# Performance work log

Measured on AMD Instinct MI355X. Metric: run time of the kernel, lower is better.

Reference implementation:

```python
import jax, jax.numpy as jnp
import numpy as np

EMB = 768
HEADS = 12
HEAD_DIM = EMB // HEADS


def setup_inputs() -> dict:
    key = jax.random.key(0)
    k1, k2, k3, k4 = jax.random.split(key, 4)
    x = jax.random.normal(k1, (8, 1024, EMB), dtype=jnp.float32)
    # Dense kernels, TF default glorot-ish scale approximated with small normals
    w_qkv = jax.random.normal(k2, (EMB, 3 * EMB), dtype=jnp.float32) * 0.02
    w_out = jax.random.normal(k3, (EMB, EMB), dtype=jnp.float32) * 0.02
    b_out = jnp.zeros((EMB,), dtype=jnp.float32)
    return {"x": x, "w_qkv": w_qkv, "w_out": w_out, "b_out": b_out}


def reference(x, w_qkv, w_out, b_out):
    B, S, E = x.shape
    qkv = jnp.einsum("bse,ef->bsf", x, w_qkv)                 # [B,S,3E]
    qkv = qkv.reshape(B, S, 3, HEADS, HEAD_DIM)
    qkv = jnp.transpose(qkv, (2, 0, 3, 1, 4))                  # [3,B,H,S,D]
    q, k, v = qkv[0], qkv[1], qkv[2]
    scale = jnp.float32(HEAD_DIM) ** -0.5
    # Blocked loop in source computes exact full (non-causal) attention:
    # every query block attends to all keys -> equivalent to standard SDPA.
    scores = jnp.einsum("bhqd,bhkd->bhqk", q, k) * scale       # [B,H,S,S]
    probs = jax.nn.softmax(scores, axis=-1)
    out = jnp.einsum("bhqk,bhkd->bhqd", probs, v)              # [B,H,S,D]
    out = jnp.transpose(out, (0, 2, 1, 3)).reshape(B, S, E)
    return jnp.einsum("bse,ef->bsf", out, w_out) + b_out
```

## Files before the change

### kernel.cpp

```cpp
#include <hip/hip_runtime.h>

typedef float f32x4 __attribute__((ext_vector_type(4)));
typedef short bf16x8 __attribute__((ext_vector_type(8)));

#define MFMA_BF16(a, b, c) __builtin_amdgcn_mfma_f32_16x16x32_bf16((a), (b), (c), 0, 0, 0)

#define GLDS16(gp, lp) __builtin_amdgcn_global_load_lds( \
    (const __attribute__((address_space(1))) unsigned int*)(gp), \
    (__attribute__((address_space(3))) unsigned int*)(lp), 16, 0, 0)

__device__ __forceinline__ ushort f2bf(float f) {
    unsigned int u = __float_as_uint(f);
    return (ushort)((u + 0x7FFFu + ((u >> 16) & 1u)) >> 16);
}

__device__ __forceinline__ float fexp2(float x) {
#if __has_builtin(__builtin_amdgcn_exp2f)
    return __builtin_amdgcn_exp2f(x);
#else
    return exp2f(x);
#endif
}

__global__ __launch_bounds__(256) void cvt_x_kernel(const float4* __restrict__ src,
                                                    ushort4* __restrict__ dst, int n4) {
    for (int i = blockIdx.x * 256 + threadIdx.x; i < n4; i += gridDim.x * 256) {
        float4 v = src[i];
        ushort4 o;
        o.x = f2bf(v.x); o.y = f2bf(v.y); o.z = f2bf(v.z); o.w = f2bf(v.w);
        dst[i] = o;
    }
}

__global__ __launch_bounds__(256) void tcvt_kernel(const float* __restrict__ src,
                                                   ushort* __restrict__ dst, int K, int N) {
    __shared__ float tile[32][33];
    const int n0 = blockIdx.x * 32, k0 = blockIdx.y * 32;
    const int c = threadIdx.x & 31, rb = threadIdx.x >> 5;
    #pragma unroll
    for (int i = 0; i < 4; ++i)
        tile[i * 8 + rb][c] = src[(size_t)(k0 + i * 8 + rb) * N + n0 + c];
    __syncthreads();
    #pragma unroll
    for (int i = 0; i < 4; ++i) {
        int nr = i * 8 + rb;
        dst[(size_t)(n0 + nr) * K + k0 + c] = f2bf(tile[c][nr]);
    }
}

__global__ __launch_bounds__(256) void gemm_qkv_mfma(
    const ushort* __restrict__ A, const ushort* __restrict__ Bt,
    ushort* __restrict__ Qo, ushort* __restrict__ Ko, ushort* __restrict__ Vo)
{
    __shared__ ushort Al[2][4096];
    __shared__ ushort Bl[2][4096];
    const int tid = threadIdx.x, lane = tid & 63;
    const int wv = tid >> 6, lo = lane & 15, hi = lane >> 4;
    const int wr = wv >> 1, wc = wv & 1;
    const int n0 = blockIdx.x * 128, m0 = blockIdx.y * 128;

    auto stage = [&](int bi, int k0) {
        #pragma unroll
        for (int it = 0; it < 2; ++it) {
            const int p = it * 256 + tid;
            const int row = p >> 2, ch = (p & 3) ^ ((row >> 1) & 3);
            GLDS16(A + (size_t)(m0 + row) * 768 + k0 + ch * 8, &Al[bi][(it * 256 + (tid & 192)) * 8]);
            GLDS16(Bt + (size_t)(n0 + row) * 768 + k0 + ch * 8, &Bl[bi][(it * 256 + (tid & 192)) * 8]);
        }
    };

    f32x4 acc[4][4];
    #pragma unroll
    for (int i = 0; i < 4; ++i)
        #pragma unroll
        for (int j = 0; j < 4; ++j)
            acc[i][j] = (f32x4){0.f, 0.f, 0.f, 0.f};

    stage(0, 0);
    __syncthreads();
    for (int kt = 0; kt < 24; ++kt) {
        const int cur = kt & 1;
        if (kt < 23) stage(cur ^ 1, (kt + 1) * 32);
        bf16x8 af[4], bfr[4];
        #pragma unroll
        for (int i = 0; i < 4; ++i) {
            const int ra = wr * 64 + i * 16 + lo;
            af[i] = *(const bf16x8*)&Al[cur][ra * 32 + ((hi ^ ((ra >> 1) & 3)) * 8)];
            const int rb = wc * 64 + i * 16 + lo;
            bfr[i] = *(const bf16x8*)&Bl[cur][rb * 32 + ((hi ^ ((rb >> 1) & 3)) * 8)];
        }
        #pragma unroll
        for (int mi = 0; mi < 4; ++mi)
            #pragma unroll
            for (int nj = 0; nj < 4; ++nj)
                acc[mi][nj] = MFMA_BF16(af[mi], bfr[nj], acc[mi][nj]);
        __syncthreads();
    }

    const int region = n0 / 768;
    const int h = ((n0 % 768) >> 6) + wc;
    if (region == 2) {
        #pragma unroll
        for (int mi = 0; mi < 4; ++mi) {
            const int m4 = m0 + wr * 64 + mi * 16 + hi * 4;
            const int b = m4 >> 10, s = m4 & 1023;
            #pragma unroll
            for (int nj = 0; nj < 4; ++nj) {
                const int d = nj * 16 + lo;
                ushort4 pk;
                pk.x = f2bf(acc[mi][nj][0]); pk.y = f2bf(acc[mi][nj][1]);
                pk.z = f2bf(acc[mi][nj][2]); pk.w = f2bf(acc[mi][nj][3]);
                *(ushort4*)&Vo[((size_t)(b * 12 + h) * 64 + d) * 1024 + s] = pk;
            }
        }
    } else {
        ushort* dst = region ? Ko : Qo;
        const float sc = region ? 1.0f : 0.18033688011112042f;
        #pragma unroll
        for (int mi = 0; mi < 4; ++mi)
            #pragma unroll
            for (int r = 0; r < 4; ++r) {
                const int m = m0 + wr * 64 + mi * 16 + hi * 4 + r;
                const int b = m >> 10, s = m & 1023;
                #pragma unroll
                for (int nj = 0; nj < 4; ++nj)
                    dst[((size_t)(b * 12 + h) * 1024 + s) * 64 + nj * 16 + lo] =
                        f2bf(acc[mi][nj][r] * sc);
            }
    }
}

__global__ __launch_bounds__(256) void attn_mfma_kernel(
    const ushort* __restrict__ Qg, const ushort* __restrict__ Kg,
    const ushort* __restrict__ Vg, ushort* __restrict__ AO)
{
    __shared__ ushort Kl[2][4096];
    __shared__ ushort Vl[2][4096];
    __shared__ ushort Pl[4][32 * 72];

    const int tid = threadIdx.x, lane = tid & 63;
    const int wv = tid >> 6, lo = lane & 15, hi = lane >> 4;
    const int L = blockIdx.x;
    const int xcd = L & 7, g = L >> 3;
    const int qb = g / 12;
    const int bh = xcd * 12 + (g % 12);
    const int b = bh / 12, h = bh % 12;
    const size_t kvbase = (size_t)bh * (1024 * 64);

    bf16x8 qa[2][2];
    const int qrow0 = qb * 128 + wv * 32;
    #pragma unroll
    for (int mi = 0; mi < 2; ++mi)
        #pragma unroll
        for (int ks = 0; ks < 2; ++ks)
            qa[mi][ks] = *(const bf16x8*)&Qg[kvbase + (size_t)(qrow0 + mi * 16 + lo) * 64 + ks * 32 + hi * 8];

    f32x4 o[2][4];
    float lp[2][4];
    #pragma unroll
    for (int mi = 0; mi < 2; ++mi) {
        #pragma unroll
        for (int dj = 0; dj < 4; ++dj) o[mi][dj] = (f32x4){0.f, 0.f, 0.f, 0.f};
        #pragma unroll
        for (int r = 0; r < 4; ++r) lp[mi][r] = 0.f;
    }

    auto stage = [&](int bi, int kt) {
        #pragma unroll
        for (int it = 0; it < 2; ++it) {
            const int p = it * 256 + tid;
            const int row = p >> 3, ch = (p & 7) ^ (row & 7);
            GLDS16(Kg + kvbase + (size_t)(kt + row) * 64 + ch * 8, &Kl[bi][(it * 256 + (tid & 192)) * 8]);
        }
        #pragma unroll
        for (int it = 0; it < 2; ++it) {
            const int p = it * 256 + tid;
            const int row = p >> 3, ch = (p & 7) ^ (row & 7);
            GLDS16(Vg + kvbase + (size_t)row * 1024 + kt + ch * 8, &Vl[bi][(it * 256 + (tid & 192)) * 8]);
        }
    };

    stage(0, 0);
    __syncthreads();

    for (int t = 0; t < 16; ++t) {
        const int cur = t & 1;
        if (t < 15) stage(cur ^ 1, (t + 1) * 64);

        f32x4 s[2][4];
        #pragma unroll
        for (int mi = 0; mi < 2; ++mi)
            #pragma unroll
            for (int nj = 0; nj < 4; ++nj) s[mi][nj] = (f32x4){0.f, 0.f, 0.f, 0.f};
        #pragma unroll
        for (int ks = 0; ks < 2; ++ks) {
            bf16x8 kb[4];
            #pragma unroll
            for (int nj = 0; nj < 4; ++nj) {
                const int key = nj * 16 + lo, c = ks * 4 + hi;
                kb[nj] = *(const bf16x8*)&Kl[cur][key * 64 + ((c ^ (key & 7)) * 8)];
            }
            #pragma unroll
            for (int mi = 0; mi < 2; ++mi)
                #pragma unroll
                for (int nj = 0; nj < 4; ++nj)
                    s[mi][nj] = MFMA_BF16(qa[mi][ks], kb[nj], s[mi][nj]);
        }

        #pragma unroll
        for (int mi = 0; mi < 2; ++mi) {
            #pragma unroll
            for (int r = 0; r < 4; ++r) {
                const unsigned int u0 = __float_as_uint(fexp2(s[mi][0][r]));
                const unsigned int u1 = __float_as_uint(fexp2(s[mi][1][r]));
                const unsigned int u2 = __float_as_uint(fexp2(s[mi][2][r]));
                const unsigned int u3 = __float_as_uint(fexp2(s[mi][3][r]));
                const float t0 = __uint_as_float(u0 & 0xFFFF0000u);
                const float t1 = __uint_as_float(u1 & 0xFFFF0000u);
                const float t2 = __uint_as_float(u2 & 0xFFFF0000u);
                const float t3 = __uint_as_float(u3 & 0xFFFF0000u);
                lp[mi][r] += (t0 + t1) + (t2 + t3);
                const int prow = mi * 16 + hi * 4 + r;
                Pl[wv][prow * 72 +      lo] = (ushort)(u0 >> 16);
                Pl[wv][prow * 72 + 16 + lo] = (ushort)(u1 >> 16);
                Pl[wv][prow * 72 + 32 + lo] = (ushort)(u2 >> 16);
                Pl[wv][prow * 72 + 48 + lo] = (ushort)(u3 >> 16);
            }
        }

        #pragma unroll
        for (int ks = 0; ks < 2; ++ks) {
            bf16x8 pa[2];
            #pragma unroll
            for (int mi = 0; mi < 2; ++mi)
                pa[mi] = *(const bf16x8*)&Pl[wv][(mi * 16 + lo) * 72 + ks * 32 + hi * 8];
            bf16x8 vb[4];
            #pragma unroll
            for (int dj = 0; dj < 4; ++dj) {
                const int d = dj * 16 + lo, c = ks * 4 + hi;
                vb[dj] = *(const bf16x8*)&Vl[cur][d * 64 + ((c ^ (d & 7)) * 8)];
            }
            #pragma unroll
            for (int mi = 0; mi < 2; ++mi)
                #pragma unroll
                for (int dj = 0; dj < 4; ++dj)
                    o[mi][dj] = MFMA_BF16(pa[mi], vb[dj], o[mi][dj]);
        }
        __syncthreads();
    }

    #pragma unroll
    for (int mi = 0; mi < 2; ++mi)
        #pragma unroll
        for (int r = 0; r < 4; ++r) {
            float l = lp[mi][r];
            l += __shfl_xor(l, 1, 16);
            l += __shfl_xor(l, 2, 16);
            l += __shfl_xor(l, 4, 16);
            l += __shfl_xor(l, 8, 16);
            const float rcp = 1.0f / l;
            const int srow = qrow0 + mi * 16 + hi * 4 + r;
            #pragma unroll
            for (int dj = 0; dj < 4; ++dj)
                AO[((size_t)(b * 1024 + srow)) * 768 + h * 64 + dj * 16 + lo] =
                    f2bf(o[mi][dj][r] * rcp);
        }
}

__global__ __launch_bounds__(256) void gemm_out_mfma(
    const ushort* __restrict__ A, const ushort* __restrict__ Bt,
    const float* __restrict__ bias, float* __restrict__ C)
{
    __shared__ ushort Al[2][4096];
    __shared__ ushort Bl[2][4096];
    const int tid = threadIdx.x, lane = tid & 63;
    const int wv = tid >> 6, lo = lane & 15, hi = lane >> 4;
    const int wr = wv >> 1, wc = wv & 1;
    const int n0 = blockIdx.x * 128, m0 = blockIdx.y * 128;

    auto stage = [&](int bi, int k0) {
        #pragma unroll
        for (int it = 0; it < 2; ++it) {
            const int p = it * 256 + tid;
            const int row = p >> 2, ch = (p & 3) ^ ((row >> 1) & 3);
            GLDS16(A + (size_t)(m0 + row) * 768 + k0 + ch * 8, &Al[bi][(it * 256 + (tid & 192)) * 8]);
            GLDS16(Bt + (size_t)(n0 + row) * 768 + k0 + ch * 8, &Bl[bi][(it * 256 + (tid & 192)) * 8]);
        }
    };

    f32x4 acc[4][4];
    #pragma unroll
    for (int i = 0; i < 4; ++i)
        #pragma unroll
        for (int j = 0; j < 4; ++j)
            acc[i][j] = (f32x4){0.f, 0.f, 0.f, 0.f};

    stage(0, 0);
    __syncthreads();
    for (int kt = 0; kt < 24; ++kt) {
        const int cur = kt & 1;
        if (kt < 23) stage(cur ^ 1, (kt + 1) * 32);
        bf16x8 af[4], bfr[4];
        #pragma unroll
        for (int i = 0; i < 4; ++i) {
            const int ra = wr * 64 + i * 16 + lo;
            af[i] = *(const bf16x8*)&Al[cur][ra * 32 + ((hi ^ ((ra >> 1) & 3)) * 8)];
            const int rb = wc * 64 + i * 16 + lo;
            bfr[i] = *(const bf16x8*)&Bl[cur][rb * 32 + ((hi ^ ((rb >> 1) & 3)) * 8)];
        }
        #pragma unroll
        for (int mi = 0; mi < 4; ++mi)
            #pragma unroll
            for (int nj = 0; nj < 4; ++nj)
                acc[mi][nj] = MFMA_BF16(af[mi], bfr[nj], acc[mi][nj]);
        __syncthreads();
    }

    const int ncol0 = n0 + wc * 64;
    float bv[4];
    #pragma unroll
    for (int nj = 0; nj < 4; ++nj) bv[nj] = bias[ncol0 + nj * 16 + lo];
    #pragma unroll
    for (int mi = 0; mi < 4; ++mi)
        #pragma unroll
        for (int r = 0; r < 4; ++r) {
            const int m = m0 + wr * 64 + mi * 16 + hi * 4 + r;
            #pragma unroll
            for (int nj = 0; nj < 4; ++nj)
                C[(size_t)m * 768 + ncol0 + nj * 16 + lo] = acc[mi][nj][r] + bv[nj];
        }
}

extern "C" void kernel_launch(void* const* d_in, const int* in_sizes, int n_in,
                              void* d_out, int out_size, void* d_ws, size_t ws_size,
                              hipStream_t stream) {
    const float* x     = (const float*)d_in[0];
    const float* w_qkv = (const float*)d_in[1];
    const float* w_out = (const float*)d_in[2];
    const float* b_out = (const float*)d_in[3];
    float* out = (float*)d_out;

    (void)in_sizes; (void)n_in; (void)out_size; (void)ws_size;

    ushort* xb   = (ushort*)d_ws;
    ushort* wqbt = xb + 6291456;
    ushort* wobt = wqbt + 1769472;
    ushort* Qs   = wobt + 589824;
    ushort* Ks   = Qs + 6291456;
    ushort* Vt   = Ks + 6291456;
    ushort* AO   = Vt + 6291456;

    cvt_x_kernel<<<2048, 256, 0, stream>>>((const float4*)x, (ushort4*)xb, 1572864);
    tcvt_kernel<<<dim3(72, 24), 256, 0, stream>>>(w_qkv, wqbt, 768, 2304);
    tcvt_kernel<<<dim3(24, 24), 256, 0, stream>>>(w_out, wobt, 768, 768);
    gemm_qkv_mfma<<<dim3(18, 64), 256, 0, stream>>>(xb, wqbt, Qs, Ks, Vt);
    attn_mfma_kernel<<<768, 256, 0, stream>>>(Qs, Ks, Vt, AO);
    gemm_out_mfma<<<dim3(6, 64), 256, 0, stream>>>(AO, wobt, b_out, out);
}
```

Measured before the change: 132.8 us.

## Swap MFMA operands for transposed accumulators, vectorize stores, remap blocks across XCDs

```diff
diff --git a/kernel.cpp b/kernel.cpp
--- a/kernel.cpp
+++ b/kernel.cpp
@@ -57,7 +57,9 @@
     const int tid = threadIdx.x, lane = tid & 63;
     const int wv = tid >> 6, lo = lane & 15, hi = lane >> 4;
     const int wr = wv >> 1, wc = wv & 1;
-    const int n0 = blockIdx.x * 128, m0 = blockIdx.y * 128;
+    const int L = blockIdx.x + 18 * blockIdx.y;
+    const int nid = (L & 7) * 144 + (L >> 3);
+    const int n0 = (nid % 18) * 128, m0 = (nid / 18) * 128;
 
     auto stage = [&](int bi, int k0) {
         #pragma unroll
@@ -76,30 +78,31 @@
         for (int j = 0; j < 4; ++j)
             acc[i][j] = (f32x4){0.f, 0.f, 0.f, 0.f};
 
+    const int region = n0 / 768;
+    const int h = ((n0 % 768) >> 6) + wc;
+
     stage(0, 0);
     __syncthreads();
-    for (int kt = 0; kt < 24; ++kt) {
-        const int cur = kt & 1;
-        if (kt < 23) stage(cur ^ 1, (kt + 1) * 32);
-        bf16x8 af[4], bfr[4];
-        #pragma unroll
-        for (int i = 0; i < 4; ++i) {
-            const int ra = wr * 64 + i * 16 + lo;
-            af[i] = *(const bf16x8*)&Al[cur][ra * 32 + ((hi ^ ((ra >> 1) & 3)) * 8)];
-            const int rb = wc * 64 + i * 16 + lo;
-            bfr[i] = *(const bf16x8*)&Bl[cur][rb * 32 + ((hi ^ ((rb >> 1) & 3)) * 8)];
-        }
-        #pragma unroll
-        for (int mi = 0; mi < 4; ++mi)
-            #pragma unroll
-            for (int nj = 0; nj < 4; ++nj)
-                acc[mi][nj] = MFMA_BF16(af[mi], bfr[nj], acc[mi][nj]);
-        __syncthreads();
-    }
-
-    const int region = n0 / 768;
-    const int h = ((n0 % 768) >> 6) + wc;
+
     if (region == 2) {
+        for (int kt = 0; kt < 24; ++kt) {
+            const int cur = kt & 1;
+            if (kt < 23) stage(cur ^ 1, (kt + 1) * 32);
+            bf16x8 af[4], bfr[4];
+            #pragma unroll
+            for (int i = 0; i < 4; ++i) {
+                const int ra = wr * 64 + i * 16 + lo;
+                af[i] = *(const bf16x8*)&Al[cur][ra * 32 + ((hi ^ ((ra >> 1) & 3)) * 8)];
+                const int rb = wc * 64 + i * 16 + lo;
+                bfr[i] = *(const bf16x8*)&Bl[cur][rb * 32 + ((hi ^ ((rb >> 1) & 3)) * 8)];
+            }
+            #pragma unroll
+            for (int mi = 0; mi < 4; ++mi)
+                #pragma unroll
+                for (int nj = 0; nj < 4; ++nj)
+                    acc[mi][nj] = MFMA_BF16(af[mi], bfr[nj], acc[mi][nj]);
+            __syncthreads();
+        }
         #pragma unroll
         for (int mi = 0; mi < 4; ++mi) {
             const int m4 = m0 + wr * 64 + mi * 16 + hi * 4;
@@ -114,19 +117,39 @@
             }
         }
     } else {
+        for (int kt = 0; kt < 24; ++kt) {
+            const int cur = kt & 1;
+            if (kt < 23) stage(cur ^ 1, (kt + 1) * 32);
+            bf16x8 af[4], bfr[4];
+            #pragma unroll
+            for (int i = 0; i < 4; ++i) {
+                const int ra = wr * 64 + i * 16 + lo;
+                af[i] = *(const bf16x8*)&Al[cur][ra * 32 + ((hi ^ ((ra >> 1) & 3)) * 8)];
+                const int rb = wc * 64 + i * 16 + lo;
+                bfr[i] = *(const bf16x8*)&Bl[cur][rb * 32 + ((hi ^ ((rb >> 1) & 3)) * 8)];
+            }
+            #pragma unroll
+            for (int mi = 0; mi < 4; ++mi)
+                #pragma unroll
+                for (int nj = 0; nj < 4; ++nj)
+                    acc[mi][nj] = MFMA_BF16(bfr[nj], af[mi], acc[mi][nj]);
+            __syncthreads();
+        }
         ushort* dst = region ? Ko : Qo;
         const float sc = region ? 1.0f : 0.18033688011112042f;
         #pragma unroll
-        for (int mi = 0; mi < 4; ++mi)
-            #pragma unroll
-            for (int r = 0; r < 4; ++r) {
-                const int m = m0 + wr * 64 + mi * 16 + hi * 4 + r;
-                const int b = m >> 10, s = m & 1023;
-                #pragma unroll
-                for (int nj = 0; nj < 4; ++nj)
-                    dst[((size_t)(b * 12 + h) * 1024 + s) * 64 + nj * 16 + lo] =
-                        f2bf(acc[mi][nj][r] * sc);
-            }
+        for (int mi = 0; mi < 4; ++mi) {
+            const int s_idx = m0 + wr * 64 + mi * 16 + lo;
+            const int b = s_idx >> 10, s = s_idx & 1023;
+            const size_t base = ((size_t)(b * 12 + h) * 1024 + s) * 64;
+            #pragma unroll
+            for (int nj = 0; nj < 4; ++nj) {
+                ushort4 pk;
+                pk.x = f2bf(acc[mi][nj][0] * sc); pk.y = f2bf(acc[mi][nj][1] * sc);
+                pk.z = f2bf(acc[mi][nj][2] * sc); pk.w = f2bf(acc[mi][nj][3] * sc);
+                *(ushort4*)&dst[base + nj * 16 + hi * 4] = pk;
+            }
+        }
     }
 }
 
@@ -156,14 +179,11 @@
             qa[mi][ks] = *(const bf16x8*)&Qg[kvbase + (size_t)(qrow0 + mi * 16 + lo) * 64 + ks * 32 + hi * 8];
 
     f32x4 o[2][4];
-    float lp[2][4];
-    #pragma unroll
-    for (int mi = 0; mi < 2; ++mi) {
+    float lp[2] = {0.f, 0.f};
+    #pragma unroll
+    for (int mi = 0; mi < 2; ++mi)
         #pragma unroll
         for (int dj = 0; dj < 4; ++dj) o[mi][dj] = (f32x4){0.f, 0.f, 0.f, 0.f};
-        #pragma unroll
-        for (int r = 0; r < 4; ++r) lp[mi][r] = 0.f;
-    }
 
     auto stage = [&](int bi, int kt) {
         #pragma unroll
@@ -204,27 +224,26 @@
             for (int mi = 0; mi < 2; ++mi)
                 #pragma unroll
                 for (int nj = 0; nj < 4; ++nj)
-                    s[mi][nj] = MFMA_BF16(qa[mi][ks], kb[nj], s[mi][nj]);
+                    s[mi][nj] = MFMA_BF16(kb[nj], qa[mi][ks], s[mi][nj]);
         }
 
         #pragma unroll
         for (int mi = 0; mi < 2; ++mi) {
             #pragma unroll
-            for (int r = 0; r < 4; ++r) {
-                const unsigned int u0 = __float_as_uint(fexp2(s[mi][0][r]));
-                const unsigned int u1 = __float_as_uint(fexp2(s[mi][1][r]));
-                const unsigned int u2 = __float_as_uint(fexp2(s[mi][2][r]));
-                const unsigned int u3 = __float_as_uint(fexp2(s[mi][3][r]));
+            for (int nj = 0; nj < 4; ++nj) {
+                const unsigned int u0 = __float_as_uint(fexp2(s[mi][nj][0]));
+                const unsigned int u1 = __float_as_uint(fexp2(s[mi][nj][1]));
+                const unsigned int u2 = __float_as_uint(fexp2(s[mi][nj][2]));
+                const unsigned int u3 = __float_as_uint(fexp2(s[mi][nj][3]));
                 const float t0 = __uint_as_float(u0 & 0xFFFF0000u);
                 const float t1 = __uint_as_float(u1 & 0xFFFF0000u);
                 const float t2 = __uint_as_float(u2 & 0xFFFF0000u);
                 const float t3 = __uint_as_float(u3 & 0xFFFF0000u);
-                lp[mi][r] += (t0 + t1) + (t2 + t3);
-                const int prow = mi * 16 + hi * 4 + r;
-                Pl[wv][prow * 72 +      lo] = (ushort)(u0 >> 16);
-                Pl[wv][prow * 72 + 16 + lo] = (ushort)(u1 >> 16);
-                Pl[wv][prow * 72 + 32 + lo] = (ushort)(u2 >> 16);
-                Pl[wv][prow * 72 + 48 + lo] = (ushort)(u3 >> 16);
+                lp[mi] += (t0 + t1) + (t2 + t3);
+                ushort4 pk;
+                pk.x = (ushort)(u0 >> 16); pk.y = (ushort)(u1 >> 16);
+                pk.z = (ushort)(u2 >> 16); pk.w = (ushort)(u3 >> 16);
+                *(ushort4*)&Pl[wv][(mi * 16 + lo) * 72 + nj * 16 + hi * 4] = pk;
             }
         }
 
@@ -250,21 +269,21 @@
     }
 
     #pragma unroll
-    for (int mi = 0; mi < 2; ++mi)
+    for (int mi = 0; mi < 2; ++mi) {
+        float l = lp[mi];
+        l += __shfl_xor(l, 16);
+        l += __shfl_xor(l, 32);
         #pragma unroll
         for (int r = 0; r < 4; ++r) {
-            float l = lp[mi][r];
-            l += __shfl_xor(l, 1, 16);
-            l += __shfl_xor(l, 2, 16);
-            l += __shfl_xor(l, 4, 16);
-            l += __shfl_xor(l, 8, 16);
-            const float rcp = 1.0f / l;
+            const float lr = __shfl(l, hi * 4 + r, 16);
+            const float rcp = 1.0f / lr;
             const int srow = qrow0 + mi * 16 + hi * 4 + r;
             #pragma unroll
             for (int dj = 0; dj < 4; ++dj)
                 AO[((size_t)(b * 1024 + srow)) * 768 + h * 64 + dj * 16 + lo] =
                     f2bf(o[mi][dj][r] * rcp);
         }
+    }
 }
 
 __global__ __launch_bounds__(256) void gemm_out_mfma(
@@ -276,7 +295,9 @@
     const int tid = threadIdx.x, lane = tid & 63;
     const int wv = tid >> 6, lo = lane & 15, hi = lane >> 4;
     const int wr = wv >> 1, wc = wv & 1;
-    const int n0 = blockIdx.x * 128, m0 = blockIdx.y * 128;
+    const int L = blockIdx.x + 6 * blockIdx.y;
+    const int nid = (L & 7) * 48 + (L >> 3);
+    const int n0 = (nid % 6) * 128, m0 = (nid / 6) * 128;
 
     auto stage = [&](int bi, int k0) {
         #pragma unroll
@@ -312,23 +333,24 @@
         for (int mi = 0; mi < 4; ++mi)
             #pragma unroll
             for (int nj = 0; nj < 4; ++nj)
-                acc[mi][nj] = MFMA_BF16(af[mi], bfr[nj], acc[mi][nj]);
+                acc[mi][nj] = MFMA_BF16(bfr[nj], af[mi], acc[mi][nj]);
         __syncthreads();
     }
 
     const int ncol0 = n0 + wc * 64;
-    float bv[4];
-    #pragma unroll
-    for (int nj = 0; nj < 4; ++nj) bv[nj] = bias[ncol0 + nj * 16 + lo];
-    #pragma unroll
-    for (int mi = 0; mi < 4; ++mi)
-        #pragma unroll
-        for (int r = 0; r < 4; ++r) {
-            const int m = m0 + wr * 64 + mi * 16 + hi * 4 + r;
-            #pragma unroll
-            for (int nj = 0; nj < 4; ++nj)
-                C[(size_t)m * 768 + ncol0 + nj * 16 + lo] = acc[mi][nj][r] + bv[nj];
-        }
+    #pragma unroll
+    for (int mi = 0; mi < 4; ++mi) {
+        const int m = m0 + wr * 64 + mi * 16 + lo;
+        #pragma unroll
+        for (int nj = 0; nj < 4; ++nj) {
+            const int nb = ncol0 + nj * 16 + hi * 4;
+            const float4 bv = *reinterpret_cast<const float4*>(&bias[nb]);
+            float4 ov;
+            ov.x = acc[mi][nj][0] + bv.x; ov.y = acc[mi][nj][1] + bv.y;
+            ov.z = acc[mi][nj][2] + bv.z; ov.w = acc[mi][nj][3] + bv.w;
+            *reinterpret_cast<float4*>(&C[(size_t)m * 768 + nb]) = ov;
+        }
+    }
 }
 
 extern "C" void kernel_launch(void* const* d_in, const int* in_sizes, int n_in,
```

After: 131.6 us. Within noise of the previous version (-0.9%).
